# Kernel optimization log

Hardware: AMD Instinct MI355X
Metric: run time of the kernel (lower is better)

Reference implementation:

```python
import jax, jax.numpy as jnp
import numpy as np

N_NODES = 50000
N_EDGES = 1600000
F_IN = 128
DIM = 128
BN_EPS = 1e-5


def setup_inputs() -> dict:
    key = jax.random.key(0)
    ks = jax.random.split(key, 8)
    x = jax.random.normal(ks[0], (N_NODES, F_IN), dtype=jnp.float32)
    edge_index = jax.random.randint(ks[1], (2, N_EDGES), 0, N_NODES, dtype=jnp.int64)
    s1 = 1.0 / np.sqrt(F_IN)
    s2 = 1.0 / np.sqrt(DIM)
    return {
        "x": x,
        "edge_index": edge_index,
        "w11": jax.random.normal(ks[2], (F_IN, DIM), dtype=jnp.float32) * s1,
        "b11": jnp.zeros((DIM,), jnp.float32),
        "w12": jax.random.normal(ks[3], (DIM, DIM), dtype=jnp.float32) * s2,
        "b12": jnp.zeros((DIM,), jnp.float32),
        "g1": jnp.ones((DIM,), jnp.float32),
        "be1": jnp.zeros((DIM,), jnp.float32),
        "w21": jax.random.normal(ks[4], (DIM, DIM), dtype=jnp.float32) * s2,
        "b21": jnp.zeros((DIM,), jnp.float32),
        "w22": jax.random.normal(ks[5], (DIM, 2), dtype=jnp.float32) * s2,
        "b22": jnp.zeros((2,), jnp.float32),
        "g2": jnp.ones((2,), jnp.float32),
        "be2": jnp.zeros((2,), jnp.float32),
    }


def _gin_conv(x, edge_index, w1, b1, w2, b2):
    # GINConv, eps=0: nn(x + sum_{(s,d) in E} x[s] scattered to d)
    src, dst = edge_index[0], edge_index[1]
    agg = jax.ops.segment_sum(x[src], dst, num_segments=N_NODES)
    h = x + agg
    h = jax.nn.relu(h @ w1 + b1)
    return h @ w2 + b2


def _batchnorm(x, gamma, beta):
    # training-mode BatchNorm1d: batch mean, biased variance, eps=1e-5
    mean = jnp.mean(x, axis=0)
    var = jnp.mean((x - mean) ** 2, axis=0)
    return (x - mean) * jax.lax.rsqrt(var + BN_EPS) * gamma + beta


def reference(x, edge_index, w11, b11, w12, b12, g1, be1,
              w21, b21, w22, b22, g2, be2):
    h = jax.nn.relu(_gin_conv(x, edge_index, w11, b11, w12, b12))
    h = _batchnorm(h, g1, be1)
    h = jax.nn.relu(_gin_conv(h, edge_index, w21, b21, w22, b22))
    h = _batchnorm(h, g2, be2)
    return h
```

## Files before the change

kernel.cpp:

```cpp
#include <hip/hip_runtime.h>

#define N_NODES 50000
#define BN_EPS 1e-5f
#define NBUCK 391
#define NCHUNK 1000
#define ENTCAP 5120

using short8 = __attribute__((ext_vector_type(8))) short;
using f32x4  = __attribute__((ext_vector_type(4))) float;

__device__ __forceinline__ float b2f(ushort h) { return __uint_as_float(((uint)h) << 16); }
__device__ __forceinline__ float blo(uint v) { return __uint_as_float(v << 16); }
__device__ __forceinline__ float bhi(uint v) { return __uint_as_float(v & 0xffff0000u); }
__device__ __forceinline__ ushort f2b(float f) {
    uint u = __float_as_uint(f);
    u += 0x7FFF + ((u >> 16) & 1);
    return (ushort)(u >> 16);
}
__device__ __forceinline__ uint packb(float lo, float hi) {
    return ((uint)f2b(hi) << 16) | (uint)f2b(lo);
}
__device__ __forceinline__ int xcd_chunk(int bid) {
    return (bid & 7) * (NCHUNK / 8) + (bid >> 3);
}

__global__ __launch_bounds__(256) void zero4_kernel(float4* __restrict__ p, int n4) {
    int i = blockIdx.x * 256 + threadIdx.x;
    if (i < n4) p[i] = make_float4(0.f, 0.f, 0.f, 0.f);
}

__global__ __launch_bounds__(256) void convert_x_kernel(const float4* __restrict__ x4,
                                                        ushort4* __restrict__ xb, int n4) {
    int i = blockIdx.x * 256 + threadIdx.x;
    if (i < n4) {
        float4 v = x4[i];
        ushort4 o;
        o.x = f2b(v.x); o.y = f2b(v.y); o.z = f2b(v.z); o.w = f2b(v.w);
        xb[i] = o;
    }
}

__global__ __launch_bounds__(256) void convert_w_kernel(const float* __restrict__ w0,
                                                        const float* __restrict__ w1,
                                                        const float* __restrict__ w2,
                                                        ushort* __restrict__ o0,
                                                        ushort* __restrict__ o1,
                                                        ushort* __restrict__ o2) {
    const float* W = (blockIdx.y == 0) ? w0 : (blockIdx.y == 1) ? w1 : w2;
    ushort* O = (blockIdx.y == 0) ? o0 : (blockIdx.y == 1) ? o1 : o2;
    int id = blockIdx.x * 256 + threadIdx.x;
    int k = id >> 7, n = id & 127;
    O[n * 128 + k] = f2b(W[id]);
}

__global__ __launch_bounds__(256) void hist_pass_kernel(const int* __restrict__ dst, int nE,
                                                        int chunk, int* __restrict__ histT) {
    __shared__ int h[NBUCK];
    for (int i = threadIdx.x; i < NBUCK; i += 256) h[i] = 0;
    __syncthreads();
    const int c = xcd_chunk(blockIdx.x);
    const int lo = c * chunk, hi = min(lo + chunk, nE);
    for (int i = lo + threadIdx.x; i < hi; i += 256) atomicAdd(&h[dst[i] >> 7], 1);
    __syncthreads();
    for (int b = threadIdx.x; b < NBUCK; b += 256) histT[b * NCHUNK + c] = h[b];
}

__global__ __launch_bounds__(256) void tot_kernel(const int* __restrict__ histT,
                                                  int* __restrict__ tot) {
    __shared__ int s[256];
    int acc = 0;
    for (int i = threadIdx.x; i < NCHUNK; i += 256) acc += histT[blockIdx.x * NCHUNK + i];
    s[threadIdx.x] = acc;
    __syncthreads();
    for (int d = 128; d > 0; d >>= 1) {
        if (threadIdx.x < d) s[threadIdx.x] += s[threadIdx.x + d];
        __syncthreads();
    }
    if (threadIdx.x == 0) tot[blockIdx.x] = s[0];
}

__global__ __launch_bounds__(1024) void base_scan_kernel(const int* __restrict__ tot,
                                                         const int* __restrict__ histT,
                                                         int* __restrict__ base_bc,
                                                         int* __restrict__ bucketbase,
                                                         int* __restrict__ rowptr, int nE) {
    __shared__ int s[1024];
    const int b = blockIdx.x;
    const int t = threadIdx.x;
    int acc = 0;
    for (int i = t; i < b; i += 1024) acc += tot[i];
    s[t] = acc;
    __syncthreads();
    for (int d = 512; d > 0; d >>= 1) {
        if (t < d) s[t] += s[t + d];
        __syncthreads();
    }
    const int bbase = s[0];
    __syncthreads();
    int v = (t < NCHUNK) ? histT[b * NCHUNK + t] : 0;
    s[t] = v;
    __syncthreads();
    for (int d = 1; d < 1024; d <<= 1) {
        int u = (t >= d) ? s[t - d] : 0;
        __syncthreads();
        s[t] += u;
        __syncthreads();
    }
    if (t < NCHUNK) base_bc[b * NCHUNK + t] = bbase + s[t] - v;
    if (t == 0) {
        bucketbase[b] = bbase;
        if (b == NBUCK - 1) bucketbase[NBUCK] = bbase + tot[b];
        if (b == 0) rowptr[N_NODES] = nE;
    }
}

__global__ __launch_bounds__(256) void place_kernel(const int* __restrict__ src,
                                                    const int* __restrict__ dst, int nE,
                                                    int chunk,
                                                    const int* __restrict__ base_bc,
                                                    uint* __restrict__ bdata) {
    __shared__ int off[NBUCK];
    const int c = xcd_chunk(blockIdx.x);
    for (int i = threadIdx.x; i < NBUCK; i += 256) off[i] = base_bc[i * NCHUNK + c];
    __syncthreads();
    const int lo = c * chunk, hi = min(lo + chunk, nE);
    for (int i = lo + threadIdx.x; i < hi; i += 256) {
        int s = src[i], d = dst[i];
        int pos = atomicAdd(&off[d >> 7], 1);
        bdata[pos] = ((uint)(d & 127) << 16) | (uint)s;
    }
}

__global__ __launch_bounds__(256) void csr_build_kernel(const int* __restrict__ bucketbase,
                                                        const uint* __restrict__ bdata,
                                                        int* __restrict__ rowptr,
                                                        ushort* __restrict__ perm, int M) {
    __shared__ uint ent[ENTCAP];
    __shared__ int hist[128];
    __shared__ int scn[128];
    __shared__ int cur[128];
    const int b = blockIdx.x;
    const int tid = threadIdx.x;
    const int bb = bucketbase[b];
    const int nb = min(bucketbase[b + 1] - bb, ENTCAP);
    if (tid < 128) hist[tid] = 0;
    for (int i = tid; i < nb; i += 256) ent[i] = bdata[bb + i];
    __syncthreads();
    for (int i = tid; i < nb; i += 256) atomicAdd(&hist[ent[i] >> 16], 1);
    __syncthreads();
    if (tid < 128) scn[tid] = hist[tid];
    __syncthreads();
    for (int d = 1; d < 128; d <<= 1) {
        int v = 0;
        if (tid < 128 && tid >= d) v = scn[tid - d];
        __syncthreads();
        if (tid < 128) scn[tid] += v;
        __syncthreads();
    }
    if (tid < 128) {
        int ex = scn[tid] - hist[tid];
        cur[tid] = ex;
        int node = b * 128 + tid;
        if (node < M) rowptr[node] = bb + ex;
    }
    __syncthreads();
    for (int i = tid; i < nb; i += 256) {
        uint e = ent[i];
        int lp = atomicAdd(&cur[e >> 16], 1);
        perm[bb + lp] = (ushort)(e & 0xffffu);
    }
}

template<bool BN>
__global__ __launch_bounds__(256) void gather_kernel(const uint4* __restrict__ xb,
                                                     const int* __restrict__ rowptr,
                                                     const ushort* __restrict__ perm,
                                                     const float* __restrict__ ss,
                                                     uint4* __restrict__ out, int M) {
    const int node = blockIdx.x * 4 + (threadIdx.x >> 6);
    if (node >= M) return;
    const int lane = threadIdx.x & 63;
    const int g = lane >> 4;
    const int r = lane & 15;
    float acc[8];
    if (g == 0) {
        uint4 v = xb[node * 16 + r];
        acc[0] = blo(v.x); acc[1] = bhi(v.x);
        acc[2] = blo(v.y); acc[3] = bhi(v.y);
        acc[4] = blo(v.z); acc[5] = bhi(v.z);
        acc[6] = blo(v.w); acc[7] = bhi(v.w);
    } else {
        #pragma unroll
        for (int k = 0; k < 8; ++k) acc[k] = 0.f;
    }
    const int beg = rowptr[node], end = rowptr[node + 1];
    int e = beg + g;
    while (e + 4 < end) {
        int s0 = perm[e];
        int s1 = perm[e + 4];
        uint4 v0 = xb[s0 * 16 + r];
        uint4 v1 = xb[s1 * 16 + r];
        acc[0] += blo(v0.x); acc[1] += bhi(v0.x);
        acc[2] += blo(v0.y); acc[3] += bhi(v0.y);
        acc[4] += blo(v0.z); acc[5] += bhi(v0.z);
        acc[6] += blo(v0.w); acc[7] += bhi(v0.w);
        acc[0] += blo(v1.x); acc[1] += bhi(v1.x);
        acc[2] += blo(v1.y); acc[3] += bhi(v1.y);
        acc[4] += blo(v1.z); acc[5] += bhi(v1.z);
        acc[6] += blo(v1.w); acc[7] += bhi(v1.w);
        e += 8;
    }
    if (e < end) {
        uint4 v0 = xb[(int)perm[e] * 16 + r];
        acc[0] += blo(v0.x); acc[1] += bhi(v0.x);
        acc[2] += blo(v0.y); acc[3] += bhi(v0.y);
        acc[4] += blo(v0.z); acc[5] += bhi(v0.z);
        acc[6] += blo(v0.w); acc[7] += bhi(v0.w);
    }
    #pragma unroll
    for (int k = 0; k < 8; ++k) {
        acc[k] += __shfl_xor(acc[k], 16);
        acc[k] += __shfl_xor(acc[k], 32);
    }
    if (g == 0) {
        if (BN) {
            const int f0 = r * 8;
            const float deg1 = (float)(end - beg + 1);
            #pragma unroll
            for (int k = 0; k < 8; ++k)
                acc[k] = acc[k] * ss[f0 + k] + deg1 * ss[128 + f0 + k];
        }
        uint4 o;
        o.x = packb(acc[0], acc[1]);
        o.y = packb(acc[2], acc[3]);
        o.z = packb(acc[4], acc[5]);
        o.w = packb(acc[6], acc[7]);
        out[node * 16 + r] = o;
    }
}

__global__ __launch_bounds__(256) void mfma_mm_kernel(const ushort* __restrict__ A,
                                                      const ushort* __restrict__ Wt,
                                                      const float* __restrict__ b,
                                                      ushort* __restrict__ C, int M) {
    const int wid = threadIdx.x >> 6;
    const int lane = threadIdx.x & 63;
    const int row0 = blockIdx.x * 64 + wid * 16;
    const int r = lane & 15;
    const int kg = lane >> 4;

    const int arow = min(row0 + r, M - 1);
    const ushort* Arow = A + (size_t)arow * 128 + kg * 8;
    short8 a[4];
    #pragma unroll
    for (int kb = 0; kb < 4; ++kb)
        a[kb] = *(const short8*)(Arow + kb * 32);

    #pragma unroll
    for (int c = 0; c < 8; ++c) {
        f32x4 acc = {0.f, 0.f, 0.f, 0.f};
        const ushort* Wcol = Wt + (size_t)(c * 16 + r) * 128 + kg * 8;
        #pragma unroll
        for (int kb = 0; kb < 4; ++kb) {
            short8 bb = *(const short8*)(Wcol + kb * 32);
            acc = __builtin_amdgcn_mfma_f32_16x16x32_bf16(a[kb], bb, acc, 0, 0, 0);
        }
        float bias = b[c * 16 + r];
        #pragma unroll
        for (int j = 0; j < 4; ++j) {
            int orow = row0 + kg * 4 + j;
            if (orow < M) {
                float v = fmaxf(acc[j] + bias, 0.f);
                C[(size_t)orow * 128 + c * 16 + r] = f2b(v);
            }
        }
    }
}

__global__ __launch_bounds__(256) void mm2_fused_kernel(const ushort* __restrict__ A,
                                                        const ushort* __restrict__ Wt,
                                                        const float* __restrict__ b1,
                                                        const float* __restrict__ W22,
                                                        const float* __restrict__ b22,
                                                        float* __restrict__ h2,
                                                        float* __restrict__ pblk, int M) {
    __shared__ float bred[4][4];
    const int wid = threadIdx.x >> 6;
    const int lane = threadIdx.x & 63;
    const int row0 = blockIdx.x * 64 + wid * 16;
    const int r = lane & 15;
    const int kg = lane >> 4;

    const int arow = min(row0 + r, M - 1);
    const ushort* Arow = A + (size_t)arow * 128 + kg * 8;
    short8 a[4];
    #pragma unroll
    for (int kb = 0; kb < 4; ++kb)
        a[kb] = *(const short8*)(Arow + kb * 32);

    float w2a[8], w2b[8];
    #pragma unroll
    for (int c = 0; c < 8; ++c) {
        w2a[c] = W22[(c * 16 + r) * 2 + 0];
        w2b[c] = W22[(c * 16 + r) * 2 + 1];
    }

    float s0[4] = {0.f, 0.f, 0.f, 0.f};
    float s1[4] = {0.f, 0.f, 0.f, 0.f};
    #pragma unroll
    for (int c = 0; c < 8; ++c) {
        f32x4 acc = {0.f, 0.f, 0.f, 0.f};
        const ushort* Wcol = Wt + (size_t)(c * 16 + r) * 128 + kg * 8;
        #pragma unroll
        for (int kb = 0; kb < 4; ++kb) {
            short8 bb = *(const short8*)(Wcol + kb * 32);
            acc = __builtin_amdgcn_mfma_f32_16x16x32_bf16(a[kb], bb, acc, 0, 0, 0);
        }
        float bias = b1[c * 16 + r];
        #pragma unroll
        for (int j = 0; j < 4; ++j) {
            int orow = row0 + kg * 4 + j;
            float v = fmaxf(acc[j] + bias, 0.f);
            if (orow >= M) v = 0.f;
            s0[j] += v * w2a[c];
            s1[j] += v * w2b[c];
        }
    }
    #pragma unroll
    for (int j = 0; j < 4; ++j) {
        #pragma unroll
        for (int d = 1; d < 16; d <<= 1) {
            s0[j] += __shfl_xor(s0[j], d);
            s1[j] += __shfl_xor(s1[j], d);
        }
    }
    float bs[4] = {0.f, 0.f, 0.f, 0.f};
    if (r == 0) {
        const float bb0 = b22[0], bb1 = b22[1];
        #pragma unroll
        for (int j = 0; j < 4; ++j) {
            int orow = row0 + kg * 4 + j;
            if (orow < M) {
                float o0 = fmaxf(s0[j] + bb0, 0.f);
                float o1 = fmaxf(s1[j] + bb1, 0.f);
                h2[(size_t)orow * 2 + 0] = o0;
                h2[(size_t)orow * 2 + 1] = o1;
                bs[0] += o0; bs[1] += o1; bs[2] += o0 * o0; bs[3] += o1 * o1;
            }
        }
    }
    #pragma unroll
    for (int k = 0; k < 4; ++k) {
        bs[k] += __shfl_xor(bs[k], 16);
        bs[k] += __shfl_xor(bs[k], 32);
    }
    if (lane == 0) {
        #pragma unroll
        for (int k = 0; k < 4; ++k) bred[wid][k] = bs[k];
    }
    __syncthreads();
    if (threadIdx.x < 4)
        pblk[(size_t)blockIdx.x * 4 + threadIdx.x] =
            bred[0][threadIdx.x] + bred[1][threadIdx.x] + bred[2][threadIdx.x] + bred[3][threadIdx.x];
}

__global__ __launch_bounds__(256) void stats128_kernel(const ushort* __restrict__ h, int M,
                                                       float* __restrict__ stats) {
    __shared__ float ssum[256];
    __shared__ float ssq[256];
    const int tid = threadIdx.x;
    const int col = tid & 127;
    float sum = 0.f, sq = 0.f;
    for (int row = blockIdx.x * 2 + (tid >> 7); row < M; row += gridDim.x * 2) {
        float v = b2f(h[(size_t)row * 128 + col]);
        sum += v; sq += v * v;
    }
    ssum[tid] = sum; ssq[tid] = sq;
    __syncthreads();
    if (tid < 128) { ssum[tid] += ssum[tid + 128]; ssq[tid] += ssq[tid + 128]; }
    __syncthreads();
    if (tid < 128) {
        atomicAdd(&stats[tid], ssum[tid]);
        atomicAdd(&stats[128 + tid], ssq[tid]);
    }
}

__global__ __launch_bounds__(256) void bn_finalize128_kernel(float* __restrict__ ss,
                                                             const float* __restrict__ g,
                                                             const float* __restrict__ be,
                                                             float invM) {
    int c = threadIdx.x;
    if (c < 128) {
        float mean = ss[c] * invM;
        float var = ss[128 + c] * invM - mean * mean;
        float sc = rsqrtf(var + BN_EPS) * g[c];
        ss[c] = sc;
        ss[128 + c] = be[c] - mean * sc;
    }
}

__global__ __launch_bounds__(256) void fin2_kernel(const float* __restrict__ pblk, int nblk,
                                                   const float* __restrict__ g,
                                                   const float* __restrict__ be,
                                                   float* __restrict__ stats, float invM) {
    __shared__ float red[256][4];
    const int tid = threadIdx.x;
    float s[4] = {0.f, 0.f, 0.f, 0.f};
    for (int b = tid; b < nblk; b += 256) {
        #pragma unroll
        for (int k = 0; k < 4; ++k) s[k] += pblk[(size_t)b * 4 + k];
    }
    #pragma unroll
    for (int k = 0; k < 4; ++k) red[tid][k] = s[k];
    __syncthreads();
    for (int d = 128; d > 0; d >>= 1) {
        if (tid < d) {
            #pragma unroll
            for (int k = 0; k < 4; ++k) red[tid][k] += red[tid + d][k];
        }
        __syncthreads();
    }
    if (tid == 0) {
        float m0 = red[0][0] * invM, m1 = red[0][1] * invM;
        float v0 = red[0][2] * invM - m0 * m0, v1 = red[0][3] * invM - m1 * m1;
        float sc0 = rsqrtf(v0 + BN_EPS) * g[0], sc1 = rsqrtf(v1 + BN_EPS) * g[1];
        stats[0] = sc0;
        stats[1] = sc1;
        stats[2] = be[0] - m0 * sc0;
        stats[3] = be[1] - m1 * sc1;
    }
}

__global__ __launch_bounds__(256) void bn_apply2_kernel(const float* __restrict__ h,
                                                        const float* __restrict__ stats,
                                                        float* __restrict__ y, int n4) {
    float sc0 = stats[0], sc1 = stats[1], sh0 = stats[2], sh1 = stats[3];
    int gid = blockIdx.x * 256 + threadIdx.x;
    if (gid >= n4) return;
    float4 v = ((const float4*)h)[gid];
    float4 o;
    o.x = v.x * sc0 + sh0;
    o.y = v.y * sc1 + sh1;
    o.z = v.z * sc0 + sh0;
    o.w = v.w * sc1 + sh1;
    ((float4*)y)[gid] = o;
}

extern "C" void kernel_launch(void* const* d_in, const int* in_sizes, int n_in,
                              void* d_out, int out_size, void* d_ws, size_t ws_size,
                              hipStream_t stream) {
    const float* x   = (const float*)d_in[0];
    const int*   ei  = (const int*)d_in[1];
    const float* w11 = (const float*)d_in[2];
    const float* b11 = (const float*)d_in[3];
    const float* w12 = (const float*)d_in[4];
    const float* b12 = (const float*)d_in[5];
    const float* g1  = (const float*)d_in[6];
    const float* be1 = (const float*)d_in[7];
    const float* w21 = (const float*)d_in[8];
    const float* b21 = (const float*)d_in[9];
    const float* w22 = (const float*)d_in[10];
    const float* b22 = (const float*)d_in[11];
    const float* g2  = (const float*)d_in[12];
    const float* be2 = (const float*)d_in[13];

    const int M  = N_NODES;
    const int nE = in_sizes[1] / 2;
    const int* src = ei;
    const int* dst = ei + nE;
    const int chunk = (nE + NCHUNK - 1) / NCHUNK;
    const int nblk = (M + 63) / 64;

    const size_t RB = (size_t)50048 * 128 * 2;
    char* p = (char*)d_ws;
    ushort* xb   = (ushort*)p;  p += RB;
    ushort* gbuf = (ushort*)p;  p += RB;
    ushort* tbuf = (ushort*)p;  p += RB;
    ushort* hbuf = (ushort*)p;  p += RB;
    float*  h2   = (float*)p;   p += 400128;
    ushort* wt11 = (ushort*)p;  p += 32768;
    ushort* wt12 = (ushort*)p;  p += 32768;
    ushort* wt21 = (ushort*)p;  p += 32768;
    float* stats1= (float*)p;   p += 256 * 4;
    float* stats2= (float*)p;   p += 16 * 4;
    float* pblk  = (float*)p;   p += (size_t)nblk * 4 * 4 + 64;
    int*  histT  = (int*)p;     p += (size_t)NBUCK * NCHUNK * 4;
    int*  base_bc= (int*)p;     p += (size_t)NBUCK * NCHUNK * 4;
    int*  tot    = (int*)p;     p += 512 * 4;
    int*  bktbase= (int*)p;     p += 512 * 4;
    int*  rowptr = (int*)p;     p += (size_t)(M + 8) * 4;
    ushort* perm = (ushort*)p;  p += (size_t)nE * 2 + 64;
    uint*  bdata = (uint*)p;

    const float invM = 1.0f / (float)M;

    zero4_kernel<<<1, 256, 0, stream>>>((float4*)stats1, 68);
    convert_x_kernel<<<(M * 32 + 255) / 256, 256, 0, stream>>>((const float4*)x, (ushort4*)xb, M * 32);
    convert_w_kernel<<<dim3(64, 3), 256, 0, stream>>>(w11, w12, w21, wt11, wt12, wt21);
    hist_pass_kernel<<<NCHUNK, 256, 0, stream>>>(dst, nE, chunk, histT);
    tot_kernel<<<NBUCK, 256, 0, stream>>>(histT, tot);
    base_scan_kernel<<<NBUCK, 1024, 0, stream>>>(tot, histT, base_bc, bktbase, rowptr, nE);
    place_kernel<<<NCHUNK, 256, 0, stream>>>(src, dst, nE, chunk, base_bc, bdata);
    csr_build_kernel<<<NBUCK, 256, 0, stream>>>(bktbase, bdata, rowptr, perm, M);

    gather_kernel<false><<<(M + 3) / 4, 256, 0, stream>>>((const uint4*)xb, rowptr, perm, nullptr, (uint4*)gbuf, M);
    mfma_mm_kernel<<<nblk, 256, 0, stream>>>(gbuf, wt11, b11, tbuf, M);
    mfma_mm_kernel<<<nblk, 256, 0, stream>>>(tbuf, wt12, b12, hbuf, M);
    stats128_kernel<<<512, 256, 0, stream>>>(hbuf, M, stats1);
    bn_finalize128_kernel<<<1, 256, 0, stream>>>(stats1, g1, be1, invM);

    gather_kernel<true><<<(M + 3) / 4, 256, 0, stream>>>((const uint4*)hbuf, rowptr, perm, stats1, (uint4*)gbuf, M);
    mm2_fused_kernel<<<nblk, 256, 0, stream>>>(gbuf, wt21, b21, w22, b22, h2, pblk, M);
    fin2_kernel<<<1, 256, 0, stream>>>(pblk, nblk, g2, be2, stats2, invM);
    bn_apply2_kernel<<<(M / 2 + 255) / 256, 256, 0, stream>>>(h2, stats2, (float*)d_out, M / 2);
}
```

Baseline: 245.6 us.

## Fuse setup kernels, layer-1 MLP with BN stats, and BN finalize into consumers

Merges the histogram, x/weight conversion and stats zeroing into one setup launch. Fuses the two layer-1 matmuls into one kernel that keeps the intermediate in LDS and accumulates BatchNorm sums into 8 replicated slots with atomics, so the separate stats pass and the tbuf round trip are gone. BN finalize steps are folded into the gather and apply kernels (each block recomputes the scale and shift), and the gather loop is unrolled to four loads in flight. This cuts launches and memory traffic, at the cost of redundant per-block reductions and atomic contention.

```diff
diff --git a/kernel.cpp b/kernel.cpp
--- a/kernel.cpp
+++ b/kernel.cpp
@@ -24,45 +24,49 @@
     return (bid & 7) * (NCHUNK / 8) + (bid >> 3);
 }
 
-__global__ __launch_bounds__(256) void zero4_kernel(float4* __restrict__ p, int n4) {
-    int i = blockIdx.x * 256 + threadIdx.x;
-    if (i < n4) p[i] = make_float4(0.f, 0.f, 0.f, 0.f);
-}
-
-__global__ __launch_bounds__(256) void convert_x_kernel(const float4* __restrict__ x4,
-                                                        ushort4* __restrict__ xb, int n4) {
-    int i = blockIdx.x * 256 + threadIdx.x;
-    if (i < n4) {
+#define B_CX 6250
+#define B_CW 192
+#define B_Z  8
+__global__ __launch_bounds__(256) void setup_kernel(const int* __restrict__ dst, int nE, int chunk,
+                                                    int* __restrict__ histT,
+                                                    const float4* __restrict__ x4,
+                                                    ushort4* __restrict__ xb,
+                                                    const float* __restrict__ w11,
+                                                    const float* __restrict__ w12,
+                                                    const float* __restrict__ w21,
+                                                    ushort* __restrict__ o11,
+                                                    ushort* __restrict__ o12,
+                                                    ushort* __restrict__ o21,
+                                                    float* __restrict__ statsrep) {
+    __shared__ int h[NBUCK];
+    const int b = blockIdx.x;
+    const int tid = threadIdx.x;
+    if (b < NCHUNK) {
+        for (int i = tid; i < NBUCK; i += 256) h[i] = 0;
+        __syncthreads();
+        const int c = xcd_chunk(b);
+        const int lo = c * chunk, hi = min(lo + chunk, nE);
+        for (int i = lo + tid; i < hi; i += 256) atomicAdd(&h[dst[i] >> 7], 1);
+        __syncthreads();
+        for (int k = tid; k < NBUCK; k += 256) histT[k * NCHUNK + c] = h[k];
+    } else if (b < NCHUNK + B_CX) {
+        int i = (b - NCHUNK) * 256 + tid;
         float4 v = x4[i];
         ushort4 o;
         o.x = f2b(v.x); o.y = f2b(v.y); o.z = f2b(v.z); o.w = f2b(v.w);
         xb[i] = o;
-    }
-}
-
-__global__ __launch_bounds__(256) void convert_w_kernel(const float* __restrict__ w0,
-                                                        const float* __restrict__ w1,
-                                                        const float* __restrict__ w2,
-                                                        ushort* __restrict__ o0,
-                                                        ushort* __restrict__ o1,
-                                                        ushort* __restrict__ o2) {
-    const float* W = (blockIdx.y == 0) ? w0 : (blockIdx.y == 1) ? w1 : w2;
-    ushort* O = (blockIdx.y == 0) ? o0 : (blockIdx.y == 1) ? o1 : o2;
-    int id = blockIdx.x * 256 + threadIdx.x;
-    int k = id >> 7, n = id & 127;
-    O[n * 128 + k] = f2b(W[id]);
-}
-
-__global__ __launch_bounds__(256) void hist_pass_kernel(const int* __restrict__ dst, int nE,
-                                                        int chunk, int* __restrict__ histT) {
-    __shared__ int h[NBUCK];
-    for (int i = threadIdx.x; i < NBUCK; i += 256) h[i] = 0;
-    __syncthreads();
-    const int c = xcd_chunk(blockIdx.x);
-    const int lo = c * chunk, hi = min(lo + chunk, nE);
-    for (int i = lo + threadIdx.x; i < hi; i += 256) atomicAdd(&h[dst[i] >> 7], 1);
-    __syncthreads();
-    for (int b = threadIdx.x; b < NBUCK; b += 256) histT[b * NCHUNK + c] = h[b];
+    } else if (b < NCHUNK + B_CX + B_CW) {
+        int id = (b - NCHUNK - B_CX) * 256 + tid;
+        int m = id >> 14;
+        int within = id & 16383;
+        int k = within >> 7, n = within & 127;
+        const float* W = (m == 0) ? w11 : (m == 1) ? w12 : w21;
+        ushort* O = (m == 0) ? o11 : (m == 1) ? o12 : o21;
+        O[n * 128 + k] = f2b(W[within]);
+    } else {
+        int i = (b - NCHUNK - B_CX - B_CW) * 256 + tid;
+        if (i < 2048) statsrep[i] = 0.f;
+    }
 }
 
 __global__ __launch_bounds__(256) void tot_kernel(const int* __restrict__ histT,
@@ -171,19 +175,45 @@
     }
 }
 
+#define ACC4(v) { acc[0] += blo(v.x); acc[1] += bhi(v.x); \
+                  acc[2] += blo(v.y); acc[3] += bhi(v.y); \
+                  acc[4] += blo(v.z); acc[5] += bhi(v.z); \
+                  acc[6] += blo(v.w); acc[7] += bhi(v.w); }
+
 template<bool BN>
 __global__ __launch_bounds__(256) void gather_kernel(const uint4* __restrict__ xb,
                                                      const int* __restrict__ rowptr,
                                                      const ushort* __restrict__ perm,
-                                                     const float* __restrict__ ss,
+                                                     const float* __restrict__ statsrep,
+                                                     const float* __restrict__ gma,
+                                                     const float* __restrict__ bta,
+                                                     float invM,
                                                      uint4* __restrict__ out, int M) {
+    __shared__ float scs[128], shs[128];
+    if (BN) {
+        if (threadIdx.x < 128) {
+            int c = threadIdx.x;
+            float s = 0.f, q = 0.f;
+            #pragma unroll
+            for (int rep = 0; rep < 8; ++rep) {
+                s += statsrep[rep * 256 + c];
+                q += statsrep[rep * 256 + 128 + c];
+            }
+            float mean = s * invM;
+            float var = q * invM - mean * mean;
+            float sc = rsqrtf(var + BN_EPS) * gma[c];
+            scs[c] = sc;
+            shs[c] = bta[c] - mean * sc;
+        }
+        __syncthreads();
+    }
     const int node = blockIdx.x * 4 + (threadIdx.x >> 6);
     if (node >= M) return;
     const int lane = threadIdx.x & 63;
-    const int g = lane >> 4;
+    const int g4 = lane >> 4;
     const int r = lane & 15;
     float acc[8];
-    if (g == 0) {
+    if (g4 == 0) {
         uint4 v = xb[node * 16 + r];
         acc[0] = blo(v.x); acc[1] = bhi(v.x);
         acc[2] = blo(v.y); acc[3] = bhi(v.y);
@@ -194,41 +224,39 @@
         for (int k = 0; k < 8; ++k) acc[k] = 0.f;
     }
     const int beg = rowptr[node], end = rowptr[node + 1];
-    int e = beg + g;
-    while (e + 4 < end) {
-        int s0 = perm[e];
-        int s1 = perm[e + 4];
+    int e = beg + g4;
+    while (e + 12 < end) {
+        int s0 = perm[e], s1 = perm[e + 4], s2 = perm[e + 8], s3 = perm[e + 12];
         uint4 v0 = xb[s0 * 16 + r];
         uint4 v1 = xb[s1 * 16 + r];
-        acc[0] += blo(v0.x); acc[1] += bhi(v0.x);
-        acc[2] += blo(v0.y); acc[3] += bhi(v0.y);
-        acc[4] += blo(v0.z); acc[5] += bhi(v0.z);
-        acc[6] += blo(v0.w); acc[7] += bhi(v0.w);
-        acc[0] += blo(v1.x); acc[1] += bhi(v1.x);
-        acc[2] += blo(v1.y); acc[3] += bhi(v1.y);
-        acc[4] += blo(v1.z); acc[5] += bhi(v1.z);
-        acc[6] += blo(v1.w); acc[7] += bhi(v1.w);
+        uint4 v2 = xb[s2 * 16 + r];
+        uint4 v3 = xb[s3 * 16 + r];
+        ACC4(v0); ACC4(v1); ACC4(v2); ACC4(v3);
+        e += 16;
+    }
+    while (e + 4 < end) {
+        int s0 = perm[e], s1 = perm[e + 4];
+        uint4 v0 = xb[s0 * 16 + r];
+        uint4 v1 = xb[s1 * 16 + r];
+        ACC4(v0); ACC4(v1);
         e += 8;
     }
     if (e < end) {
         uint4 v0 = xb[(int)perm[e] * 16 + r];
-        acc[0] += blo(v0.x); acc[1] += bhi(v0.x);
-        acc[2] += blo(v0.y); acc[3] += bhi(v0.y);
-        acc[4] += blo(v0.z); acc[5] += bhi(v0.z);
-        acc[6] += blo(v0.w); acc[7] += bhi(v0.w);
+        ACC4(v0);
     }
     #pragma unroll
     for (int k = 0; k < 8; ++k) {
         acc[k] += __shfl_xor(acc[k], 16);
         acc[k] += __shfl_xor(acc[k], 32);
     }
-    if (g == 0) {
+    if (g4 == 0) {
         if (BN) {
             const int f0 = r * 8;
             const float deg1 = (float)(end - beg + 1);
             #pragma unroll
             for (int k = 0; k < 8; ++k)
-                acc[k] = acc[k] * ss[f0 + k] + deg1 * ss[128 + f0 + k];
+                acc[k] = acc[k] * scs[f0 + k] + deg1 * shs[f0 + k];
         }
         uint4 o;
         o.x = packb(acc[0], acc[1]);
@@ -239,17 +267,21 @@
     }
 }
 
-__global__ __launch_bounds__(256) void mfma_mm_kernel(const ushort* __restrict__ A,
-                                                      const ushort* __restrict__ Wt,
-                                                      const float* __restrict__ b,
-                                                      ushort* __restrict__ C, int M) {
+__global__ __launch_bounds__(256) void mmL1_fused_kernel(const ushort* __restrict__ A,
+                                                         const ushort* __restrict__ Wt1,
+                                                         const float* __restrict__ b1,
+                                                         const ushort* __restrict__ Wt2,
+                                                         const float* __restrict__ b2,
+                                                         ushort* __restrict__ C,
+                                                         float* __restrict__ statsrep, int M) {
+    __shared__ float T[4][64][33];
     const int wid = threadIdx.x >> 6;
     const int lane = threadIdx.x & 63;
-    const int row0 = blockIdx.x * 64 + wid * 16;
+    const int row0 = blockIdx.x * 64;
     const int r = lane & 15;
     const int kg = lane >> 4;
 
-    const int arow = min(row0 + r, M - 1);
+    const int arow = min(row0 + wid * 16 + r, M - 1);
     const ushort* Arow = A + (size_t)arow * 128 + kg * 8;
     short8 a[4];
     #pragma unroll
@@ -259,20 +291,55 @@
     #pragma unroll
     for (int c = 0; c < 8; ++c) {
         f32x4 acc = {0.f, 0.f, 0.f, 0.f};
-        const ushort* Wcol = Wt + (size_t)(c * 16 + r) * 128 + kg * 8;
+        const ushort* Wcol = Wt1 + (size_t)(c * 16 + r) * 128 + kg * 8;
         #pragma unroll
         for (int kb = 0; kb < 4; ++kb) {
             short8 bb = *(const short8*)(Wcol + kb * 32);
             acc = __builtin_amdgcn_mfma_f32_16x16x32_bf16(a[kb], bb, acc, 0, 0, 0);
         }
-        float bias = b[c * 16 + r];
+        const float bias = b1[c * 16 + r];
+        const int kb_w = c >> 1;
+        const int inner = ((c & 1) << 4) + r;
+        #pragma unroll
+        for (int j = 0; j < 4; ++j)
+            T[kb_w][wid * 16 + kg * 4 + j][inner] = fmaxf(acc[j] + bias, 0.f);
+    }
+    __syncthreads();
+
+    const int lrow = wid * 16 + r;
+    short8 a2[4];
+    #pragma unroll
+    for (int kb = 0; kb < 4; ++kb) {
+        #pragma unroll
+        for (int i = 0; i < 8; ++i)
+            a2[kb][i] = (short)f2b(T[kb][lrow][kg * 8 + i]);
+    }
+
+    float* sr = statsrep + (blockIdx.x & 7) * 256;
+    #pragma unroll
+    for (int c = 0; c < 8; ++c) {
+        f32x4 acc = {0.f, 0.f, 0.f, 0.f};
+        const ushort* Wcol = Wt2 + (size_t)(c * 16 + r) * 128 + kg * 8;
+        #pragma unroll
+        for (int kb = 0; kb < 4; ++kb) {
+            short8 bb = *(const short8*)(Wcol + kb * 32);
+            acc = __builtin_amdgcn_mfma_f32_16x16x32_bf16(a2[kb], bb, acc, 0, 0, 0);
+        }
+        const float bias = b2[c * 16 + r];
+        float s = 0.f, q = 0.f;
         #pragma unroll
         for (int j = 0; j < 4; ++j) {
-            int orow = row0 + kg * 4 + j;
-            if (orow < M) {
-                float v = fmaxf(acc[j] + bias, 0.f);
-                C[(size_t)orow * 128 + c * 16 + r] = f2b(v);
-            }
+            int orow = row0 + wid * 16 + kg * 4 + j;
+            float v = fmaxf(acc[j] + bias, 0.f);
+            if (orow < M) C[(size_t)orow * 128 + c * 16 + r] = f2b(v);
+            else v = 0.f;
+            s += v; q += v * v;
+        }
+        s += __shfl_xor(s, 16); s += __shfl_xor(s, 32);
+        q += __shfl_xor(q, 16); q += __shfl_xor(q, 32);
+        if (kg == 0) {
+            atomicAdd(&sr[c * 16 + r], s);
+            atomicAdd(&sr[128 + c * 16 + r], q);
         }
     }
 }
@@ -283,7 +350,7 @@
                                                         const float* __restrict__ W22,
                                                         const float* __restrict__ b22,
                                                         float* __restrict__ h2,
-                                                        float* __restrict__ pblk, int M) {
+                                                        float4* __restrict__ pblk, int M) {
     __shared__ float bred[4][4];
     const int wid = threadIdx.x >> 6;
     const int lane = threadIdx.x & 63;
@@ -359,83 +426,42 @@
         for (int k = 0; k < 4; ++k) bred[wid][k] = bs[k];
     }
     __syncthreads();
-    if (threadIdx.x < 4)
-        pblk[(size_t)blockIdx.x * 4 + threadIdx.x] =
-            bred[0][threadIdx.x] + bred[1][threadIdx.x] + bred[2][threadIdx.x] + bred[3][threadIdx.x];
-}
-
-__global__ __launch_bounds__(256) void stats128_kernel(const ushort* __restrict__ h, int M,
-                                                       float* __restrict__ stats) {
-    __shared__ float ssum[256];
-    __shared__ float ssq[256];
+    if (threadIdx.x == 0)
+        pblk[blockIdx.x] = make_float4(bred[0][0] + bred[1][0] + bred[2][0] + bred[3][0],
+                                       bred[0][1] + bred[1][1] + bred[2][1] + bred[3][1],
+                                       bred[0][2] + bred[1][2] + bred[2][2] + bred[3][2],
+                                       bred[0][3] + bred[1][3] + bred[2][3] + bred[3][3]);
+}
+
+__global__ __launch_bounds__(256) void bn_apply2_kernel(const float* __restrict__ h,
+                                                        const float4* __restrict__ pblk, int nblk,
+                                                        const float* __restrict__ gma,
+                                                        const float* __restrict__ bta,
+                                                        float* __restrict__ y, int n4, float invM) {
+    __shared__ float4 red[256];
     const int tid = threadIdx.x;
-    const int col = tid & 127;
-    float sum = 0.f, sq = 0.f;
-    for (int row = blockIdx.x * 2 + (tid >> 7); row < M; row += gridDim.x * 2) {
-        float v = b2f(h[(size_t)row * 128 + col]);
-        sum += v; sq += v * v;
-    }
-    ssum[tid] = sum; ssq[tid] = sq;
-    __syncthreads();
-    if (tid < 128) { ssum[tid] += ssum[tid + 128]; ssq[tid] += ssq[tid + 128]; }
-    __syncthreads();
-    if (tid < 128) {
-        atomicAdd(&stats[tid], ssum[tid]);
-        atomicAdd(&stats[128 + tid], ssq[tid]);
-    }
-}
-
-__global__ __launch_bounds__(256) void bn_finalize128_kernel(float* __restrict__ ss,
-                                                             const float* __restrict__ g,
-                                                             const float* __restrict__ be,
-                                                             float invM) {
-    int c = threadIdx.x;
-    if (c < 128) {
-        float mean = ss[c] * invM;
-        float var = ss[128 + c] * invM - mean * mean;
-        float sc = rsqrtf(var + BN_EPS) * g[c];
-        ss[c] = sc;
-        ss[128 + c] = be[c] - mean * sc;
-    }
-}
-
-__global__ __launch_bounds__(256) void fin2_kernel(const float* __restrict__ pblk, int nblk,
-                                                   const float* __restrict__ g,
-                                                   const float* __restrict__ be,
-                                                   float* __restrict__ stats, float invM) {
-    __shared__ float red[256][4];
-    const int tid = threadIdx.x;
-    float s[4] = {0.f, 0.f, 0.f, 0.f};
+    float4 s = make_float4(0.f, 0.f, 0.f, 0.f);
     for (int b = tid; b < nblk; b += 256) {
-        #pragma unroll
-        for (int k = 0; k < 4; ++k) s[k] += pblk[(size_t)b * 4 + k];
-    }
-    #pragma unroll
-    for (int k = 0; k < 4; ++k) red[tid][k] = s[k];
+        float4 t = pblk[b];
+        s.x += t.x; s.y += t.y; s.z += t.z; s.w += t.w;
+    }
+    red[tid] = s;
     __syncthreads();
     for (int d = 128; d > 0; d >>= 1) {
         if (tid < d) {
-            #pragma unroll
-            for (int k = 0; k < 4; ++k) red[tid][k] += red[tid + d][k];
-        }
-        __syncthreads();
-    }
-    if (tid == 0) {
-        float m0 = red[0][0] * invM, m1 = red[0][1] * invM;
-        float v0 = red[0][2] * invM - m0 * m0, v1 = red[0][3] * invM - m1 * m1;
-        float sc0 = rsqrtf(v0 + BN_EPS) * g[0], sc1 = rsqrtf(v1 + BN_EPS) * g[1];
-        stats[0] = sc0;
-        stats[1] = sc1;
-        stats[2] = be[0] - m0 * sc0;
-        stats[3] = be[1] - m1 * sc1;
-    }
-}
-
-__global__ __launch_bounds__(256) void bn_apply2_kernel(const float* __restrict__ h,
-                                                        const float* __restrict__ stats,
-                                                        float* __restrict__ y, int n4) {
-    float sc0 = stats[0], sc1 = stats[1], sh0 = stats[2], sh1 = stats[3];
-    int gid = blockIdx.x * 256 + threadIdx.x;
+            red[tid].x += red[tid + d].x;
+            red[tid].y += red[tid + d].y;
+            red[tid].z += red[tid + d].z;
+            red[tid].w += red[tid + d].w;
+        }
+        __syncthreads();
+    }
+    const float4 tot = red[0];
+    const float m0 = tot.x * invM, m1 = tot.y * invM;
+    const float v0 = tot.z * invM - m0 * m0, v1 = tot.w * invM - m1 * m1;
+    const float sc0 = rsqrtf(v0 + BN_EPS) * gma[0], sc1 = rsqrtf(v1 + BN_EPS) * gma[1];
+    const float sh0 = bta[0] - m0 * sc0, sh1 = bta[1] - m1 * sc1;
+    int gid = blockIdx.x * 256 + tid;
     if (gid >= n4) return;
     float4 v = ((const float4*)h)[gid];
     float4 o;
@@ -475,15 +501,13 @@
     char* p = (char*)d_ws;
     ushort* xb   = (ushort*)p;  p += RB;
     ushort* gbuf = (ushort*)p;  p += RB;
-    ushort* tbuf = (ushort*)p;  p += RB;
     ushort* hbuf = (ushort*)p;  p += RB;
     float*  h2   = (float*)p;   p += 400128;
     ushort* wt11 = (ushort*)p;  p += 32768;
     ushort* wt12 = (ushort*)p;  p += 32768;
     ushort* wt21 = (ushort*)p;  p += 32768;
-    float* stats1= (float*)p;   p += 256 * 4;
-    float* stats2= (float*)p;   p += 16 * 4;
-    float* pblk  = (float*)p;   p += (size_t)nblk * 4 * 4 + 64;
+    float* statsrep = (float*)p; p += 2048 * 4;
+    float4* pblk = (float4*)p;  p += (size_t)nblk * 16 + 64;
     int*  histT  = (int*)p;     p += (size_t)NBUCK * NCHUNK * 4;
     int*  base_bc= (int*)p;     p += (size_t)NBUCK * NCHUNK * 4;
     int*  tot    = (int*)p;     p += 512 * 4;
@@ -494,23 +518,23 @@
 
     const float invM = 1.0f / (float)M;
 
-    zero4_kernel<<<1, 256, 0, stream>>>((float4*)stats1, 68);
-    convert_x_kernel<<<(M * 32 + 255) / 256, 256, 0, stream>>>((const float4*)x, (ushort4*)xb, M * 32);
-    convert_w_kernel<<<dim3(64, 3), 256, 0, stream>>>(w11, w12, w21, wt11, wt12, wt21);
-    hist_pass_kernel<<<NCHUNK, 256, 0, stream>>>(dst, nE, chunk, histT);
+    setup_kernel<<<NCHUNK + B_CX + B_CW + B_Z, 256, 0, stream>>>(
+        dst, nE, chunk, histT, (const float4*)x, (ushort4*)xb,
+        w11, w12, w21, wt11, wt12, wt21, statsrep);
     tot_kernel<<<NBUCK, 256, 0, stream>>>(histT, tot);
     base_scan_kernel<<<NBUCK, 1024, 0, stream>>>(tot, histT, base_bc, bktbase, rowptr, nE);
     place_kernel<<<NCHUNK, 256, 0, stream>>>(src, dst, nE, chunk, base_bc, bdata);
     csr_build_kernel<<<NBUCK, 256, 0, stream>>>(bktbase, bdata, rowptr, perm, M);
 
-    gather_kernel<false><<<(M + 3) / 4, 256, 0, stream>>>((const uint4*)xb, rowptr, perm, nullptr, (uint4*)gbuf, M);
-    mfma_mm_kernel<<<nblk, 256, 0, stream>>>(gbuf, wt11, b11, tbuf, M);
-    mfma_mm_kernel<<<nblk, 256, 0, stream>>>(tbuf, wt12, b12, hbuf, M);
-    stats128_kernel<<<512, 256, 0, stream>>>(hbuf, M, stats1);
-    bn_finalize128_kernel<<<1, 256, 0, stream>>>(stats1, g1, be1, invM);
-
-    gather_kernel<true><<<(M + 3) / 4, 256, 0, stream>>>((const uint4*)hbuf, rowptr, perm, stats1, (uint4*)gbuf, M);
+    gather_kernel<false><<<(M + 3) / 4, 256, 0, stream>>>((const uint4*)xb, rowptr, perm,
+                                                          nullptr, nullptr, nullptr, 0.f,
+                                                          (uint4*)gbuf, M);
+    mmL1_fused_kernel<<<nblk, 256, 0, stream>>>(gbuf, wt11, b11, wt12, b12, hbuf, statsrep, M);
+
+    gather_kernel<true><<<(M + 3) / 4, 256, 0, stream>>>((const uint4*)hbuf, rowptr, perm,
+                                                         statsrep, g1, be1, invM,
+                                                         (uint4*)gbuf, M);
     mm2_fused_kernel<<<nblk, 256, 0, stream>>>(gbuf, wt21, b21, w22, b22, h2, pblk, M);
-    fin2_kernel<<<1, 256, 0, stream>>>(pblk, nblk, g2, be2, stats2, invM);
-    bn_apply2_kernel<<<(M / 2 + 255) / 256, 256, 0, stream>>>(h2, stats2, (float*)d_out, M / 2);
-}
+    bn_apply2_kernel<<<(M / 2 + 255) / 256, 256, 0, stream>>>(h2, pblk, nblk, g2, be2,
+                                                              (float*)d_out, M / 2, invM);
+}
```

Result: faster. 216.7 us (-11.7%).
